# Kernel tuning notes

Measured on AMD Instinct MI355X. Metric: run time of the kernel, lower is better.

The kernel has to match this reference:

```python
import jax, jax.numpy as jnp
import numpy as np

N = 512        # number of evidences
D = 512        # hidden_dim

def setup_inputs() -> dict:
    key = jax.random.key(0)
    k0, k1, k2, k3, k4 = jax.random.split(key, 5)
    s = 1.0 / np.sqrt(2 * D)
    return {
        "h_e":  jax.random.normal(k0, (N, D), dtype=jnp.float32),
        "W0_w": jax.random.uniform(k1, (D, 2 * D), minval=-s, maxval=s, dtype=jnp.float32),  # nn.Linear(2d, d).weight
        "W0_b": jax.random.uniform(k2, (D,), minval=-s, maxval=s, dtype=jnp.float32),
        "W1_w": jax.random.uniform(k3, (1, D), minval=-1/np.sqrt(D), maxval=1/np.sqrt(D), dtype=jnp.float32),
        "W1_b": jax.random.uniform(k4, (1,), minval=-1/np.sqrt(D), maxval=1/np.sqrt(D), dtype=jnp.float32),
    }

def reference(h_e, W0_w, W0_b, W0b_unused=None, W1_w=None, W1_b=None):
    pass  # placeholder replaced below

def reference(h_e, W0_w, W0_b, W1_w, W1_b):
    d = h_e.shape[-1]
    # W_0([h_i ; h_j]) == h_i @ A^T + h_j @ B^T where W0_w = [A | B]
    Wa = W0_w[:, :d]          # [d, d] acts on h_i
    Wb = W0_w[:, d:]          # [d, d] acts on h_j
    pre_i = jnp.einsum('id,hd->ih', h_e, Wa)            # [n, d]
    pre_j = jnp.einsum('jd,hd->jh', h_e, Wb)            # [n, d]
    hidden = jax.nn.relu(pre_i[:, None, :] + pre_j[None, :, :] + W0_b)  # [n, n, d]
    p = jnp.einsum('ijh,oh->ijo', hidden, W1_w)[..., 0] + W1_b[0]       # [n, n]
    a = jax.nn.softmax(p, axis=-1)                                      # [n, n]
    return a @ h_e                                                      # [n, d]
```

## Files before the change

kernel.cpp:

```cpp
#include <hip/hip_runtime.h>


using bf16x8 = __attribute__((ext_vector_type(8))) short;
using f32x4  = __attribute__((ext_vector_type(4))) float;
using f16x2  = __attribute__((ext_vector_type(2))) _Float16;
using f16x8  = __attribute__((ext_vector_type(8))) _Float16;

#define SC_STR 68

__device__ __forceinline__ unsigned short f2bf(float x) {
    unsigned int u = __float_as_uint(x);
    u += 0x7fffu + ((u >> 16) & 1u);
    return (unsigned short)(u >> 16);
}

__global__ __launch_bounds__(256) void k_prep(const float* __restrict__ he,
                                              const float* __restrict__ w0,
                                              unsigned short* __restrict__ heb,
                                              unsigned short* __restrict__ hebT,
                                              unsigned short* __restrict__ w0b) {
    const int tid = threadIdx.x;
    if (blockIdx.z == 0) {
        __shared__ unsigned short T[64][65];
        const int r0 = blockIdx.y * 64, c0 = blockIdx.x * 64;
        #pragma unroll
        for (int rep = 0; rep < 4; ++rep) {
            int f = tid + rep * 256;
            int row = f >> 4, col = (f & 15) * 4;
            float4 a = *(const float4*)&he[(r0 + row) * 512 + c0 + col];
            unsigned short q0 = f2bf(a.x), q1 = f2bf(a.y), q2 = f2bf(a.z), q3 = f2bf(a.w);
            *(ushort4*)&heb[(r0 + row) * 512 + c0 + col] = make_ushort4(q0, q1, q2, q3);
            T[row][col + 0] = q0; T[row][col + 1] = q1;
            T[row][col + 2] = q2; T[row][col + 3] = q3;
        }
        __syncthreads();
        #pragma unroll
        for (int rep = 0; rep < 4; ++rep) {
            int f = tid + rep * 256;
            int trow = f >> 4, tcol = (f & 15) * 4;
            ushort4 v = make_ushort4(T[tcol + 0][trow], T[tcol + 1][trow],
                                     T[tcol + 2][trow], T[tcol + 3][trow]);
            *(ushort4*)&hebT[(c0 + trow) * 512 + r0 + tcol] = v;
        }
    } else {
        const int r0 = blockIdx.y * 64, c0 = blockIdx.x * 64 + (blockIdx.z - 1) * 512;
        #pragma unroll
        for (int rep = 0; rep < 4; ++rep) {
            int f = tid + rep * 256;
            int row = f >> 4, col = (f & 15) * 4;
            float4 a = *(const float4*)&w0[(r0 + row) * 1024 + c0 + col];
            *(ushort4*)&w0b[(r0 + row) * 1024 + c0 + col] =
                make_ushort4(f2bf(a.x), f2bf(a.y), f2bf(a.z), f2bf(a.w));
        }
    }
}

__global__ __launch_bounds__(64) void k_preA(const unsigned short* __restrict__ heb,
                                             const unsigned short* __restrict__ w0b,
                                             const float* __restrict__ b0,
                                             _Float16* __restrict__ CI,
                                             _Float16* __restrict__ CJ) {
    const int l = threadIdx.x;
    const int c0 = blockIdx.x * 32;
    const int i0 = blockIdx.y * 32;
    const int r16 = l & 15;
    const int k0l = (l >> 4) * 8;
    const int hrow0 = c0 & 511;
    const int dofs = (c0 >= 512) ? 512 : 0;

    f32x4 acc[2][2] = {};
    const unsigned short* pa0 = heb + (i0 + r16) * 512;
    const unsigned short* pa1 = heb + (i0 + 16 + r16) * 512;
    const unsigned short* pb0 = w0b + (hrow0 + r16) * 1024 + dofs;
    const unsigned short* pb1 = w0b + (hrow0 + 16 + r16) * 1024 + dofs;

    #pragma unroll
    for (int ks = 0; ks < 16; ++ks) {
        const int k0 = ks * 32 + k0l;
        bf16x8 a0 = *(const bf16x8*)(pa0 + k0);
        bf16x8 a1 = *(const bf16x8*)(pa1 + k0);
        bf16x8 b0v = *(const bf16x8*)(pb0 + k0);
        bf16x8 b1v = *(const bf16x8*)(pb1 + k0);
        acc[0][0] = __builtin_amdgcn_mfma_f32_16x16x32_bf16(a0, b0v, acc[0][0], 0, 0, 0);
        acc[0][1] = __builtin_amdgcn_mfma_f32_16x16x32_bf16(a0, b1v, acc[0][1], 0, 0, 0);
        acc[1][0] = __builtin_amdgcn_mfma_f32_16x16x32_bf16(a1, b0v, acc[1][0], 0, 0, 0);
        acc[1][1] = __builtin_amdgcn_mfma_f32_16x16x32_bf16(a1, b1v, acc[1][1], 0, 0, 0);
    }
    const int orow = (l >> 4) * 4;
    if (dofs) {
        const float bb0 = b0[hrow0 + r16];
        const float bb1 = b0[hrow0 + 16 + r16];
        #pragma unroll
        for (int ti = 0; ti < 2; ++ti)
            #pragma unroll
            for (int tj = 0; tj < 2; ++tj) {
                const float bb = tj ? bb1 : bb0;
                #pragma unroll
                for (int r = 0; r < 4; ++r)
                    CJ[(i0 + ti * 16 + orow + r) * 512 + hrow0 + tj * 16 + r16] =
                        (_Float16)(acc[ti][tj][r] + bb);
            }
    } else {
        #pragma unroll
        for (int ti = 0; ti < 2; ++ti)
            #pragma unroll
            for (int tj = 0; tj < 2; ++tj)
                #pragma unroll
                for (int r = 0; r < 4; ++r)
                    CI[(i0 + ti * 16 + orow + r) * 512 + c0 + tj * 16 + r16] =
                        (_Float16)acc[ti][tj][r];
    }
}

__global__ __launch_bounds__(256) void k_score(const _Float16* __restrict__ CI,
                                               const _Float16* __restrict__ CJ,
                                               const float* __restrict__ w1,
                                               float* __restrict__ Ppart) {
    const int tid = threadIdx.x;
    const int tx = tid & 15, ty = tid >> 4;
    const int j0 = blockIdx.x * 64;
    const int i0 = blockIdx.y * 64;
    const int hs = blockIdx.z;

    __shared__ __align__(16) f16x2 As2[16 * SC_STR];
    __shared__ __align__(16) f16x2 Bs2[16 * SC_STR];
    __shared__ f16x2 Ws2[16];

    const f16x2 fz = {(_Float16)0, (_Float16)0};
    float acc[4][4] = {};

    for (int kt = 0; kt < 2; ++kt) {
        const int hb = hs * 64 + kt * 32;
        {
            const int row = tid >> 2;
            const int hc = (tid & 3) * 8;
            const int hp = hc >> 1;
            f16x8 av = *(const f16x8*)&CI[(i0 + row) * 512 + hb + hc];
            As2[(hp + 0) * SC_STR + row] = __builtin_shufflevector(av, av, 0, 1);
            As2[(hp + 1) * SC_STR + row] = __builtin_shufflevector(av, av, 2, 3);
            As2[(hp + 2) * SC_STR + row] = __builtin_shufflevector(av, av, 4, 5);
            As2[(hp + 3) * SC_STR + row] = __builtin_shufflevector(av, av, 6, 7);
            f16x8 bv = *(const f16x8*)&CJ[(j0 + row) * 512 + hb + hc];
            Bs2[(hp + 0) * SC_STR + row] = __builtin_shufflevector(bv, bv, 0, 1);
            Bs2[(hp + 1) * SC_STR + row] = __builtin_shufflevector(bv, bv, 2, 3);
            Bs2[(hp + 2) * SC_STR + row] = __builtin_shufflevector(bv, bv, 4, 5);
            Bs2[(hp + 3) * SC_STR + row] = __builtin_shufflevector(bv, bv, 6, 7);
        }
        if (tid < 16) {
            float2 w = *(const float2*)&w1[hb + 2 * tid];
            f16x2 wp = {(_Float16)w.x, (_Float16)w.y};
            Ws2[tid] = wp;
        }
        __syncthreads();
        #pragma unroll
        for (int k = 0; k < 16; ++k) {
            f16x8 a8 = *(const f16x8*)&As2[k * SC_STR + 4 * ty];
            f16x8 b8 = *(const f16x8*)&Bs2[k * SC_STR + 4 * tx];
            const f16x2 w = Ws2[k];
            f16x2 ap[4] = { __builtin_shufflevector(a8, a8, 0, 1),
                            __builtin_shufflevector(a8, a8, 2, 3),
                            __builtin_shufflevector(a8, a8, 4, 5),
                            __builtin_shufflevector(a8, a8, 6, 7) };
            f16x2 bp[4] = { __builtin_shufflevector(b8, b8, 0, 1),
                            __builtin_shufflevector(b8, b8, 2, 3),
                            __builtin_shufflevector(b8, b8, 4, 5),
                            __builtin_shufflevector(b8, b8, 6, 7) };
            #pragma unroll
            for (int ii = 0; ii < 4; ++ii)
                #pragma unroll
                for (int jj = 0; jj < 4; ++jj) {
                    f16x2 s = ap[ii] + bp[jj];
                    s = __builtin_elementwise_max(s, fz);
                    acc[ii][jj] = __builtin_amdgcn_fdot2(s, w, acc[ii][jj], false);
                }
        }
        __syncthreads();
    }
    float* outp = Ppart + (size_t)hs * 512 * 512;
    #pragma unroll
    for (int ii = 0; ii < 4; ++ii) {
        float4 v = make_float4(acc[ii][0], acc[ii][1], acc[ii][2], acc[ii][3]);
        *(float4*)&outp[(i0 + 4 * ty + ii) * 512 + j0 + 4 * tx] = v;
    }
}

__global__ __launch_bounds__(256) void k_softmax(const float* __restrict__ Ppart,
                                                 unsigned short* __restrict__ Awb) {
    const int i = blockIdx.x;
    const int tid = threadIdx.x;
    float p0 = 0.f, p1 = 0.f;
    #pragma unroll
    for (int s = 0; s < 8; ++s) {
        p0 += Ppart[s * 262144 + i * 512 + tid];
        p1 += Ppart[s * 262144 + i * 512 + tid + 256];
    }
    __shared__ float red[256];
    red[tid] = fmaxf(p0, p1);
    __syncthreads();
    for (int s = 128; s > 0; s >>= 1) {
        if (tid < s) red[tid] = fmaxf(red[tid], red[tid + s]);
        __syncthreads();
    }
    const float m = red[0];
    __syncthreads();
    const float e0 = __expf(p0 - m);
    const float e1 = __expf(p1 - m);
    red[tid] = e0 + e1;
    __syncthreads();
    for (int s = 128; s > 0; s >>= 1) {
        if (tid < s) red[tid] += red[tid + s];
        __syncthreads();
    }
    const float inv = 1.0f / red[0];
    Awb[i * 512 + tid] = f2bf(e0 * inv);
    Awb[i * 512 + tid + 256] = f2bf(e1 * inv);
}

__global__ __launch_bounds__(64) void k_outM(const unsigned short* __restrict__ Awb,
                                             const unsigned short* __restrict__ hebT,
                                             float* __restrict__ outp) {
    const int l = threadIdx.x;
    const int d0 = blockIdx.x * 32;
    const int i0 = blockIdx.y * 16;
    const int r16 = l & 15;
    const int k0l = (l >> 4) * 8;

    f32x4 acc[2] = {};
    const unsigned short* pa  = Awb  + (i0 + r16) * 512;
    const unsigned short* pb0 = hebT + (d0 + r16) * 512;
    const unsigned short* pb1 = hebT + (d0 + 16 + r16) * 512;

    #pragma unroll
    for (int ks = 0; ks < 16; ++ks) {
        const int k0 = ks * 32 + k0l;
        bf16x8 a  = *(const bf16x8*)(pa + k0);
        bf16x8 b0 = *(const bf16x8*)(pb0 + k0);
        bf16x8 b1 = *(const bf16x8*)(pb1 + k0);
        acc[0] = __builtin_amdgcn_mfma_f32_16x16x32_bf16(a, b0, acc[0], 0, 0, 0);
        acc[1] = __builtin_amdgcn_mfma_f32_16x16x32_bf16(a, b1, acc[1], 0, 0, 0);
    }
    const int orow = (l >> 4) * 4;
    #pragma unroll
    for (int tj = 0; tj < 2; ++tj)
        #pragma unroll
        for (int r = 0; r < 4; ++r)
            outp[(i0 + orow + r) * 512 + d0 + tj * 16 + r16] = acc[tj][r];
}

extern "C" void kernel_launch(void* const* d_in, const int* in_sizes, int n_in,
                              void* d_out, int out_size, void* d_ws, size_t ws_size,
                              hipStream_t stream) {
    const float* he = (const float*)d_in[0];
    const float* w0 = (const float*)d_in[1];
    const float* b0 = (const float*)d_in[2];
    const float* w1 = (const float*)d_in[3];
    float* outp = (float*)d_out;

    float* Ppart = (float*)d_ws;
    _Float16* CI = (_Float16*)(Ppart + 8 * 512 * 512);
    _Float16* CJ = CI + 512 * 512;
    unsigned short* heb  = (unsigned short*)(CJ + 512 * 512);
    unsigned short* hebT = heb + 512 * 512;
    unsigned short* w0b  = hebT + 512 * 512;
    unsigned short* Awb  = w0b + 512 * 1024;

    k_prep   <<<dim3(8, 8, 3), 256, 0, stream>>>(he, w0, heb, hebT, w0b);
    k_preA   <<<dim3(32, 16),  64,  0, stream>>>(heb, w0b, b0, CI, CJ);
    k_score  <<<dim3(8, 8, 8), 256, 0, stream>>>(CI, CJ, w1, Ppart);
    k_softmax<<<dim3(512),     256, 0, stream>>>(Ppart, Awb);
    k_outM   <<<dim3(16, 32),  64,  0, stream>>>(Awb, hebT, outp);
}
```

Baseline: 91.89 us.

## Drop prep kernel, convert in-GEMM, retile score kernel, fold transpose into softmax

Removes the separate bf16 conversion kernel. The projection GEMM now reads fp32 inputs directly and converts them with packed bf16 conversion instructions, using 256-thread blocks of four waves. The score kernel is retiled to 32x64 output tiles over 128-wide hidden slices, which halves the number of partial-score buffers and removes the inner loop barriers. The transposed bf16 copy of h_e is now produced by the first 64 softmax blocks. Together these cut one launch and the intermediate global traffic, at the cost of redundant fp32 loads and conversions in the GEMM and a larger shared-memory footprint in the score kernel.

```diff
diff --git a/kernel.cpp b/kernel.cpp
--- a/kernel.cpp
+++ b/kernel.cpp
@@ -4,9 +4,11 @@
 using bf16x8 = __attribute__((ext_vector_type(8))) short;
 using f32x4  = __attribute__((ext_vector_type(4))) float;
 using f16x2  = __attribute__((ext_vector_type(2))) _Float16;
+using f16x4  = __attribute__((ext_vector_type(4))) _Float16;
 using f16x8  = __attribute__((ext_vector_type(8))) _Float16;
 
-#define SC_STR 68
+#define STRA 34
+#define STRB 68
 
 __device__ __forceinline__ unsigned short f2bf(float x) {
     unsigned int u = __float_as_uint(x);
@@ -14,73 +16,43 @@
     return (unsigned short)(u >> 16);
 }
 
-__global__ __launch_bounds__(256) void k_prep(const float* __restrict__ he,
+__device__ __forceinline__ bf16x8 cvt8(float4 lo, float4 hi) {
+    union { bf16x8 v; unsigned int u[4]; } r;
+    asm("v_cvt_pk_bf16_f32 %0, %1, %2" : "=v"(r.u[0]) : "v"(lo.x), "v"(lo.y));
+    asm("v_cvt_pk_bf16_f32 %0, %1, %2" : "=v"(r.u[1]) : "v"(lo.z), "v"(lo.w));
+    asm("v_cvt_pk_bf16_f32 %0, %1, %2" : "=v"(r.u[2]) : "v"(hi.x), "v"(hi.y));
+    asm("v_cvt_pk_bf16_f32 %0, %1, %2" : "=v"(r.u[3]) : "v"(hi.z), "v"(hi.w));
+    return r.v;
+}
+
+__global__ __launch_bounds__(256) void k_preA(const float* __restrict__ he,
                                               const float* __restrict__ w0,
-                                              unsigned short* __restrict__ heb,
-                                              unsigned short* __restrict__ hebT,
-                                              unsigned short* __restrict__ w0b) {
+                                              const float* __restrict__ b0,
+                                              _Float16* __restrict__ CI,
+                                              _Float16* __restrict__ CJ) {
     const int tid = threadIdx.x;
-    if (blockIdx.z == 0) {
-        __shared__ unsigned short T[64][65];
-        const int r0 = blockIdx.y * 64, c0 = blockIdx.x * 64;
-        #pragma unroll
-        for (int rep = 0; rep < 4; ++rep) {
-            int f = tid + rep * 256;
-            int row = f >> 4, col = (f & 15) * 4;
-            float4 a = *(const float4*)&he[(r0 + row) * 512 + c0 + col];
-            unsigned short q0 = f2bf(a.x), q1 = f2bf(a.y), q2 = f2bf(a.z), q3 = f2bf(a.w);
-            *(ushort4*)&heb[(r0 + row) * 512 + c0 + col] = make_ushort4(q0, q1, q2, q3);
-            T[row][col + 0] = q0; T[row][col + 1] = q1;
-            T[row][col + 2] = q2; T[row][col + 3] = q3;
-        }
-        __syncthreads();
-        #pragma unroll
-        for (int rep = 0; rep < 4; ++rep) {
-            int f = tid + rep * 256;
-            int trow = f >> 4, tcol = (f & 15) * 4;
-            ushort4 v = make_ushort4(T[tcol + 0][trow], T[tcol + 1][trow],
-                                     T[tcol + 2][trow], T[tcol + 3][trow]);
-            *(ushort4*)&hebT[(c0 + trow) * 512 + r0 + tcol] = v;
-        }
-    } else {
-        const int r0 = blockIdx.y * 64, c0 = blockIdx.x * 64 + (blockIdx.z - 1) * 512;
-        #pragma unroll
-        for (int rep = 0; rep < 4; ++rep) {
-            int f = tid + rep * 256;
-            int row = f >> 4, col = (f & 15) * 4;
-            float4 a = *(const float4*)&w0[(r0 + row) * 1024 + c0 + col];
-            *(ushort4*)&w0b[(r0 + row) * 1024 + c0 + col] =
-                make_ushort4(f2bf(a.x), f2bf(a.y), f2bf(a.z), f2bf(a.w));
-        }
-    }
-}
-
-__global__ __launch_bounds__(64) void k_preA(const unsigned short* __restrict__ heb,
-                                             const unsigned short* __restrict__ w0b,
-                                             const float* __restrict__ b0,
-                                             _Float16* __restrict__ CI,
-                                             _Float16* __restrict__ CJ) {
-    const int l = threadIdx.x;
-    const int c0 = blockIdx.x * 32;
-    const int i0 = blockIdx.y * 32;
+    const int l = tid & 63;
+    const int w = tid >> 6;
+    const int c0 = blockIdx.x * 64 + (w & 1) * 32;
+    const int i0 = blockIdx.y * 64 + (w >> 1) * 32;
     const int r16 = l & 15;
     const int k0l = (l >> 4) * 8;
     const int hrow0 = c0 & 511;
     const int dofs = (c0 >= 512) ? 512 : 0;
 
     f32x4 acc[2][2] = {};
-    const unsigned short* pa0 = heb + (i0 + r16) * 512;
-    const unsigned short* pa1 = heb + (i0 + 16 + r16) * 512;
-    const unsigned short* pb0 = w0b + (hrow0 + r16) * 1024 + dofs;
-    const unsigned short* pb1 = w0b + (hrow0 + 16 + r16) * 1024 + dofs;
+    const float* pa0 = he + (i0 + r16) * 512;
+    const float* pa1 = pa0 + 16 * 512;
+    const float* pb0 = w0 + (hrow0 + r16) * 1024 + dofs;
+    const float* pb1 = pb0 + 16 * 1024;
 
     #pragma unroll
     for (int ks = 0; ks < 16; ++ks) {
         const int k0 = ks * 32 + k0l;
-        bf16x8 a0 = *(const bf16x8*)(pa0 + k0);
-        bf16x8 a1 = *(const bf16x8*)(pa1 + k0);
-        bf16x8 b0v = *(const bf16x8*)(pb0 + k0);
-        bf16x8 b1v = *(const bf16x8*)(pb1 + k0);
+        bf16x8 a0 = cvt8(*(const float4*)(pa0 + k0), *(const float4*)(pa0 + k0 + 4));
+        bf16x8 a1 = cvt8(*(const float4*)(pa1 + k0), *(const float4*)(pa1 + k0 + 4));
+        bf16x8 b0v = cvt8(*(const float4*)(pb0 + k0), *(const float4*)(pb0 + k0 + 4));
+        bf16x8 b1v = cvt8(*(const float4*)(pb1 + k0), *(const float4*)(pb1 + k0 + 4));
         acc[0][0] = __builtin_amdgcn_mfma_f32_16x16x32_bf16(a0, b0v, acc[0][0], 0, 0, 0);
         acc[0][1] = __builtin_amdgcn_mfma_f32_16x16x32_bf16(a0, b1v, acc[0][1], 0, 0, 0);
         acc[1][0] = __builtin_amdgcn_mfma_f32_16x16x32_bf16(a1, b0v, acc[1][0], 0, 0, 0);
@@ -119,78 +91,92 @@
     const int tid = threadIdx.x;
     const int tx = tid & 15, ty = tid >> 4;
     const int j0 = blockIdx.x * 64;
-    const int i0 = blockIdx.y * 64;
-    const int hs = blockIdx.z;
-
-    __shared__ __align__(16) f16x2 As2[16 * SC_STR];
-    __shared__ __align__(16) f16x2 Bs2[16 * SC_STR];
-    __shared__ f16x2 Ws2[16];
+    const int i0 = blockIdx.y * 32;
+    const int hb = blockIdx.z * 128;
+
+    __shared__ __align__(16) f16x2 As2[64 * STRA];
+    __shared__ __align__(16) f16x2 Bs2[64 * STRB];
+    __shared__ f16x2 Ws2[64];
 
     const f16x2 fz = {(_Float16)0, (_Float16)0};
-    float acc[4][4] = {};
-
-    for (int kt = 0; kt < 2; ++kt) {
-        const int hb = hs * 64 + kt * 32;
-        {
-            const int row = tid >> 2;
-            const int hc = (tid & 3) * 8;
-            const int hp = hc >> 1;
-            f16x8 av = *(const f16x8*)&CI[(i0 + row) * 512 + hb + hc];
-            As2[(hp + 0) * SC_STR + row] = __builtin_shufflevector(av, av, 0, 1);
-            As2[(hp + 1) * SC_STR + row] = __builtin_shufflevector(av, av, 2, 3);
-            As2[(hp + 2) * SC_STR + row] = __builtin_shufflevector(av, av, 4, 5);
-            As2[(hp + 3) * SC_STR + row] = __builtin_shufflevector(av, av, 6, 7);
-            f16x8 bv = *(const f16x8*)&CJ[(j0 + row) * 512 + hb + hc];
-            Bs2[(hp + 0) * SC_STR + row] = __builtin_shufflevector(bv, bv, 0, 1);
-            Bs2[(hp + 1) * SC_STR + row] = __builtin_shufflevector(bv, bv, 2, 3);
-            Bs2[(hp + 2) * SC_STR + row] = __builtin_shufflevector(bv, bv, 4, 5);
-            Bs2[(hp + 3) * SC_STR + row] = __builtin_shufflevector(bv, bv, 6, 7);
+    float acc[2][4] = {};
+
+    {
+        const int row = tid >> 3, seg = tid & 7;
+        f16x8 v0 = *(const f16x8*)&CI[(i0 + row) * 512 + hb + seg * 16];
+        f16x8 v1 = *(const f16x8*)&CI[(i0 + row) * 512 + hb + seg * 16 + 8];
+        const int hp = seg * 8;
+        As2[(hp + 0) * STRA + row] = __builtin_shufflevector(v0, v0, 0, 1);
+        As2[(hp + 1) * STRA + row] = __builtin_shufflevector(v0, v0, 2, 3);
+        As2[(hp + 2) * STRA + row] = __builtin_shufflevector(v0, v0, 4, 5);
+        As2[(hp + 3) * STRA + row] = __builtin_shufflevector(v0, v0, 6, 7);
+        As2[(hp + 4) * STRA + row] = __builtin_shufflevector(v1, v1, 0, 1);
+        As2[(hp + 5) * STRA + row] = __builtin_shufflevector(v1, v1, 2, 3);
+        As2[(hp + 6) * STRA + row] = __builtin_shufflevector(v1, v1, 4, 5);
+        As2[(hp + 7) * STRA + row] = __builtin_shufflevector(v1, v1, 6, 7);
+    }
+    {
+        const int row = tid >> 2;
+        #pragma unroll
+        for (int s2 = 0; s2 < 2; ++s2) {
+            const int seg = (tid & 3) * 2 + s2;
+            f16x8 v0 = *(const f16x8*)&CJ[(j0 + row) * 512 + hb + seg * 16];
+            f16x8 v1 = *(const f16x8*)&CJ[(j0 + row) * 512 + hb + seg * 16 + 8];
+            const int hp = seg * 8;
+            Bs2[(hp + 0) * STRB + row] = __builtin_shufflevector(v0, v0, 0, 1);
+            Bs2[(hp + 1) * STRB + row] = __builtin_shufflevector(v0, v0, 2, 3);
+            Bs2[(hp + 2) * STRB + row] = __builtin_shufflevector(v0, v0, 4, 5);
+            Bs2[(hp + 3) * STRB + row] = __builtin_shufflevector(v0, v0, 6, 7);
+            Bs2[(hp + 4) * STRB + row] = __builtin_shufflevector(v1, v1, 0, 1);
+            Bs2[(hp + 5) * STRB + row] = __builtin_shufflevector(v1, v1, 2, 3);
+            Bs2[(hp + 6) * STRB + row] = __builtin_shufflevector(v1, v1, 4, 5);
+            Bs2[(hp + 7) * STRB + row] = __builtin_shufflevector(v1, v1, 6, 7);
         }
-        if (tid < 16) {
-            float2 w = *(const float2*)&w1[hb + 2 * tid];
-            f16x2 wp = {(_Float16)w.x, (_Float16)w.y};
-            Ws2[tid] = wp;
-        }
-        __syncthreads();
-        #pragma unroll
-        for (int k = 0; k < 16; ++k) {
-            f16x8 a8 = *(const f16x8*)&As2[k * SC_STR + 4 * ty];
-            f16x8 b8 = *(const f16x8*)&Bs2[k * SC_STR + 4 * tx];
-            const f16x2 w = Ws2[k];
-            f16x2 ap[4] = { __builtin_shufflevector(a8, a8, 0, 1),
-                            __builtin_shufflevector(a8, a8, 2, 3),
-                            __builtin_shufflevector(a8, a8, 4, 5),
-                            __builtin_shufflevector(a8, a8, 6, 7) };
-            f16x2 bp[4] = { __builtin_shufflevector(b8, b8, 0, 1),
-                            __builtin_shufflevector(b8, b8, 2, 3),
-                            __builtin_shufflevector(b8, b8, 4, 5),
-                            __builtin_shufflevector(b8, b8, 6, 7) };
+    }
+    if (tid < 64) {
+        float2 wv = *(const float2*)&w1[hb + 2 * tid];
+        f16x2 wp = {(_Float16)wv.x, (_Float16)wv.y};
+        Ws2[tid] = wp;
+    }
+    __syncthreads();
+
+    #pragma unroll 8
+    for (int k = 0; k < 64; ++k) {
+        f16x4 a4 = *(const f16x4*)&As2[k * STRA + 2 * ty];
+        f16x8 b8 = *(const f16x8*)&Bs2[k * STRB + 4 * tx];
+        const f16x2 wp = Ws2[k];
+        f16x2 ap[2] = { __builtin_shufflevector(a4, a4, 0, 1),
+                        __builtin_shufflevector(a4, a4, 2, 3) };
+        f16x2 bp[4] = { __builtin_shufflevector(b8, b8, 0, 1),
+                        __builtin_shufflevector(b8, b8, 2, 3),
+                        __builtin_shufflevector(b8, b8, 4, 5),
+                        __builtin_shufflevector(b8, b8, 6, 7) };
+        #pragma unroll
+        for (int ii = 0; ii < 2; ++ii)
             #pragma unroll
-            for (int ii = 0; ii < 4; ++ii)
-                #pragma unroll
-                for (int jj = 0; jj < 4; ++jj) {
-                    f16x2 s = ap[ii] + bp[jj];
-                    s = __builtin_elementwise_max(s, fz);
-                    acc[ii][jj] = __builtin_amdgcn_fdot2(s, w, acc[ii][jj], false);
-                }
-        }
-        __syncthreads();
-    }
-    float* outp = Ppart + (size_t)hs * 512 * 512;
-    #pragma unroll
-    for (int ii = 0; ii < 4; ++ii) {
+            for (int jj = 0; jj < 4; ++jj) {
+                f16x2 s = ap[ii] + bp[jj];
+                s = __builtin_elementwise_max(s, fz);
+                acc[ii][jj] = __builtin_amdgcn_fdot2(s, wp, acc[ii][jj], false);
+            }
+    }
+    float* outp = Ppart + (size_t)blockIdx.z * 512 * 512;
+    #pragma unroll
+    for (int ii = 0; ii < 2; ++ii) {
         float4 v = make_float4(acc[ii][0], acc[ii][1], acc[ii][2], acc[ii][3]);
-        *(float4*)&outp[(i0 + 4 * ty + ii) * 512 + j0 + 4 * tx] = v;
+        *(float4*)&outp[(i0 + 2 * ty + ii) * 512 + j0 + 4 * tx] = v;
     }
 }
 
 __global__ __launch_bounds__(256) void k_softmax(const float* __restrict__ Ppart,
-                                                 unsigned short* __restrict__ Awb) {
+                                                 const float* __restrict__ he,
+                                                 unsigned short* __restrict__ Awb,
+                                                 unsigned short* __restrict__ hebT) {
     const int i = blockIdx.x;
     const int tid = threadIdx.x;
     float p0 = 0.f, p1 = 0.f;
     #pragma unroll
-    for (int s = 0; s < 8; ++s) {
+    for (int s = 0; s < 4; ++s) {
         p0 += Ppart[s * 262144 + i * 512 + tid];
         p1 += Ppart[s * 262144 + i * 512 + tid + 256];
     }
@@ -214,6 +200,28 @@
     const float inv = 1.0f / red[0];
     Awb[i * 512 + tid] = f2bf(e0 * inv);
     Awb[i * 512 + tid + 256] = f2bf(e1 * inv);
+
+    if (i < 64) {
+        __shared__ unsigned short T[64][65];
+        const int r0 = (i >> 3) * 64, c0 = (i & 7) * 64;
+        #pragma unroll
+        for (int rep = 0; rep < 4; ++rep) {
+            int f = tid + rep * 256;
+            int row = f >> 4, col = (f & 15) * 4;
+            float4 a = *(const float4*)&he[(r0 + row) * 512 + c0 + col];
+            T[row][col + 0] = f2bf(a.x); T[row][col + 1] = f2bf(a.y);
+            T[row][col + 2] = f2bf(a.z); T[row][col + 3] = f2bf(a.w);
+        }
+        __syncthreads();
+        #pragma unroll
+        for (int rep = 0; rep < 4; ++rep) {
+            int f = tid + rep * 256;
+            int trow = f >> 4, tcol = (f & 15) * 4;
+            ushort4 v = make_ushort4(T[tcol + 0][trow], T[tcol + 1][trow],
+                                     T[tcol + 2][trow], T[tcol + 3][trow]);
+            *(ushort4*)&hebT[(c0 + trow) * 512 + r0 + tcol] = v;
+        }
+    }
 }
 
 __global__ __launch_bounds__(64) void k_outM(const unsigned short* __restrict__ Awb,
@@ -257,16 +265,13 @@
     float* outp = (float*)d_out;
 
     float* Ppart = (float*)d_ws;
-    _Float16* CI = (_Float16*)(Ppart + 8 * 512 * 512);
+    _Float16* CI = (_Float16*)(Ppart + 4 * 512 * 512);
     _Float16* CJ = CI + 512 * 512;
-    unsigned short* heb  = (unsigned short*)(CJ + 512 * 512);
-    unsigned short* hebT = heb + 512 * 512;
-    unsigned short* w0b  = hebT + 512 * 512;
-    unsigned short* Awb  = w0b + 512 * 1024;
-
-    k_prep   <<<dim3(8, 8, 3), 256, 0, stream>>>(he, w0, heb, hebT, w0b);
-    k_preA   <<<dim3(32, 16),  64,  0, stream>>>(heb, w0b, b0, CI, CJ);
-    k_score  <<<dim3(8, 8, 8), 256, 0, stream>>>(CI, CJ, w1, Ppart);
-    k_softmax<<<dim3(512),     256, 0, stream>>>(Ppart, Awb);
+    unsigned short* hebT = (unsigned short*)(CJ + 512 * 512);
+    unsigned short* Awb  = hebT + 512 * 512;
+
+    k_preA   <<<dim3(16, 8),   256, 0, stream>>>(he, w0, b0, CI, CJ);
+    k_score  <<<dim3(8, 16, 4), 256, 0, stream>>>(CI, CJ, w1, Ppart);
+    k_softmax<<<dim3(512),     256, 0, stream>>>(Ppart, he, Awb, hebT);
     k_outM   <<<dim3(16, 32),  64,  0, stream>>>(Awb, hebT, outp);
 }
```

New measurement: 97.59 us. 6.2% more time.
